# Optimization experiments

Hardware: AMD Instinct MI355X
Metric: run time of the kernel (lower is better)

The kernel has to match this reference:

```python
import jax, jax.numpy as jnp
import numpy as np

B, K, V, T, S, H = 128, 10, 50257, 20, 4, 2048  # batch, beam, vocab, seq_len, n_state, hidden


def setup_inputs() -> dict:
    key = jax.random.key(0)
    k1, k2, k3, k4, k5 = jax.random.split(key, 5)
    return {
        "logprobs": jax.random.normal(k1, (B, K, V), dtype=jnp.float32),
        "logprobs_sum": jax.random.normal(k2, (B, K), dtype=jnp.float32),
        "beam_seq_logprobs": jax.random.normal(k3, (B, T, K), dtype=jnp.float32),
        "state": jax.random.normal(k4, (B, S, K, H), dtype=jnp.float32),
        "beam_seq": jax.random.randint(k5, (B, T, K), 0, V, dtype=jnp.int64),
        "t": 5,
    }


def _beam_step(lp, lp_sum, seq, seq_lp, st, t):
    # lp: [K, V], lp_sum: [K], seq: [T, K] int, seq_lp: [T, K], st: [S, K, H]
    vocab = lp.shape[-1]
    # logprobsf[:, -1] -= 1000 (suppress EOS-like last token)
    lp = lp.at[:, vocab - 1].add(-1000.0)
    # group_size == 1 -> add_diversity is a no-op; unaug_logprobsf == lp.
    # torch.sort(logprobsf, 1, True) then take cols = beam_size per row == per-row top-k
    ys, ix = jax.lax.top_k(lp, K)  # [K(q), K(c)]
    # candidates appended with c outer, q inner -> flat index = c*K + q
    cand = lp_sum[:, None] + ys              # [q, c]
    flat = cand.T.reshape(-1)                # ordered as c*K + q
    order = jnp.argsort(-flat)[:K]           # stable descending sort, keep top beam
    c_sel = order // K
    q_sel = order % K
    tok = ix[q_sel, c_sel]                   # v['c']
    r = ys[q_sel, c_sel]                     # v['r'] (unaug == aug here)
    p = flat[order]                          # v['p']
    time_idx = jnp.arange(seq.shape[0])[:, None]
    # only rows < t are reordered from the parent beam; row t gets new entries
    new_seq = jnp.where(time_idx < t, seq[:, q_sel], seq).at[t].set(tok)
    new_seq_lp = jnp.where(time_idx < t, seq_lp[:, q_sel], seq_lp).at[t].set(r)
    new_state = st[:, q_sel, :]              # state gather/reorder on beam axis
    return new_seq, new_seq_lp, p, new_state


def reference(logprobs, logprobs_sum, beam_seq_logprobs, state, beam_seq, t):
    step = jax.vmap(_beam_step, in_axes=(0, 0, 0, 0, 0, None))
    return step(logprobs, logprobs_sum, beam_seq, beam_seq_logprobs, state, t)
```

## Files before the change

### kernel.cpp

```cpp
#include <hip/hip_runtime.h>
#include <math.h>
#include <stdint.h>

#define NB 128
#define NK 10
#define NV 50257
#define NT 20
#define NS 4
#define NH 2048

#define QCAP 576
#define QTRIG 48

__device__ __forceinline__ unsigned key_of(float f) {
    unsigned u = __float_as_uint(f);
    unsigned m = (unsigned)((int)u >> 31) | 0x80000000u;
    return u ^ m;
}
__device__ __forceinline__ float val_of(unsigned k) {
    unsigned m = (k & 0x80000000u) ? 0x80000000u : 0xFFFFFFFFu;
    return __uint_as_float(k ^ m);
}
__device__ __forceinline__ float rdlanef(float v, int l) {
    return __uint_as_float((unsigned)__builtin_amdgcn_readlane((int)__float_as_uint(v), l));
}

__global__ __launch_bounds__(256) void topk_rows(const float* __restrict__ lp,
                                                 float* __restrict__ ys,
                                                 int*   __restrict__ ix) {
    const int row  = blockIdx.x;
    const int tid  = threadIdx.x;
    const int lane = tid & 63;
    const int wave = tid >> 6;
    const float* rowp = lp + (size_t)row * NV;

    __shared__ unsigned long long Q[4][QCAP];
    __shared__ int qcnt[4];

    if (lane == 0) qcnt[wave] = 0;
    __threadfence_block();

    float thr = -INFINITY;

    auto lane_append = [&](float v, int idx) {
        if (v >= thr) {
            int p = atomicAdd(&qcnt[wave], 1);
            Q[wave][p] = ((unsigned long long)key_of(v) << 32) | (unsigned)(~(unsigned)idx);
        }
    };

    auto compact = [&]() {
        __threadfence_block();
        int cnt = qcnt[wave];
        if (cnt > 10) {
            if (cnt <= 64) {
                unsigned long long mine = (lane < cnt) ? Q[wave][lane] : 0ull;
                int rk = 0;
                for (int j = 0; j < cnt; ++j)
                    rk += (Q[wave][j] > mine) ? 1 : 0;
                __threadfence_block();
                if (lane < cnt && rk < 10) Q[wave][rk] = mine;
            } else {
                unsigned long long mine[9];
                int rk[9];
#pragma unroll
                for (int s = 0; s < 9; ++s) {
                    int e = lane + (s << 6);
                    mine[s] = (e < cnt) ? Q[wave][e] : 0ull;
                    rk[s] = 0;
                }
                for (int j = 0; j < cnt; ++j) {
                    unsigned long long qv = Q[wave][j];
#pragma unroll
                    for (int s = 0; s < 9; ++s) rk[s] += (qv > mine[s]) ? 1 : 0;
                }
                __threadfence_block();
#pragma unroll
                for (int s = 0; s < 9; ++s) {
                    int e = lane + (s << 6);
                    if (e < cnt && rk[s] < 10) Q[wave][rk[s]] = mine[s];
                }
            }
            if (lane == 0) qcnt[wave] = 10;
            __threadfence_block();
            thr = val_of((unsigned)(Q[wave][9] >> 32));
        }
    };

    auto process8 = [&](float4 a, float4 b, int basea) {
        float m8 = fmaxf(fmaxf(fmaxf(a.x, a.y), fmaxf(a.z, a.w)),
                         fmaxf(fmaxf(b.x, b.y), fmaxf(b.z, b.w)));
        if (__ballot(m8 >= thr)) {
            lane_append(a.x, basea + 0);
            lane_append(a.y, basea + 1);
            lane_append(a.z, basea + 2);
            lane_append(a.w, basea + 3);
            lane_append(b.x, basea + 1024);
            lane_append(b.y, basea + 1025);
            lane_append(b.z, basea + 1026);
            lane_append(b.w, basea + 1027);
            __threadfence_block();
            if (qcnt[wave] >= QTRIG) compact();
        }
    };

    const int head = (int)(((16u - (unsigned)((uintptr_t)rowp & 15u)) & 15u) >> 2);
    const int n4 = (NV - 1 - head) >> 2;
    const int NFULL = n4 >> 9;
    const float4* rowp4 = (const float4*)(rowp + head);

    float4 a0 = rowp4[tid];
    float4 b0 = rowp4[tid + 256];
    float4 pa = rowp4[512 + tid];
    float4 pb = rowp4[768 + tid];

    float m8 = fmaxf(fmaxf(fmaxf(a0.x, a0.y), fmaxf(a0.z, a0.w)),
                     fmaxf(fmaxf(b0.x, b0.y), fmaxf(b0.z, b0.w)));
    int rank = 0;
    for (int j = 0; j < 64; ++j) {
        float o = rdlanef(m8, j);
        rank += ((o > m8) || (o == m8 && j < lane)) ? 1 : 0;
    }
    {
        unsigned long long b9 = __ballot(rank == 9);
        int l9 = (int)__builtin_ctzll(b9);
        thr = rdlanef(m8, l9);
    }
    {
        int basea = head + 4 * tid;
        lane_append(a0.x, basea + 0);
        lane_append(a0.y, basea + 1);
        lane_append(a0.z, basea + 2);
        lane_append(a0.w, basea + 3);
        lane_append(b0.x, basea + 1024);
        lane_append(b0.y, basea + 1025);
        lane_append(b0.z, basea + 1026);
        lane_append(b0.w, basea + 1027);
        __threadfence_block();
        if (qcnt[wave] >= QTRIG) compact();
    }

    for (int it = 1; it < NFULL; ++it) {
        float4 ca = pa, cb = pb;
        int nit = (it + 1 < NFULL) ? it + 1 : it;
        pa = rowp4[(nit << 9) + tid];
        pb = rowp4[(nit << 9) + 256 + tid];
        process8(ca, cb, head + 4 * ((it << 9) + tid));
    }
    {
        int ja = (NFULL << 9) + tid;
        int jb = ja + 256;
        float4 a = (ja < n4) ? rowp4[ja]
                             : make_float4(-INFINITY, -INFINITY, -INFINITY, -INFINITY);
        float4 b = (jb < n4) ? rowp4[jb]
                             : make_float4(-INFINITY, -INFINITY, -INFINITY, -INFINITY);
        process8(a, b, head + 4 * ja);
    }
    if (wave == 0) {
        if (lane < head) lane_append(rowp[lane], lane);
        int idx = head + 4 * n4 + lane;
        if (idx < NV) {
            float v = rowp[idx];
            if (idx == NV - 1) v -= 1000.0f;
            lane_append(v, idx);
        }
    }

    compact();
    __syncthreads();

    if (tid < 40) {
        int w = tid / 10, r = tid - w * 10;
        unsigned long long my = Q[w][r];
        int rnk = 0;
#pragma unroll
        for (int w2 = 0; w2 < 4; ++w2)
            for (int r2 = 0; r2 < 10; ++r2)
                rnk += (Q[w2][r2] > my) ? 1 : 0;
        if (rnk < 10) {
            ys[row * 10 + rnk] = val_of((unsigned)(my >> 32));
            ix[row * 10 + rnk] = (int)(~(unsigned)(my & 0xFFFFFFFFull));
        }
    }
}

__global__ __launch_bounds__(128) void beam_select(
    const float* __restrict__ lp_sum,
    const float* __restrict__ seq_lp,
    const int*   __restrict__ seq,
    const int*   __restrict__ tptr,
    const float* __restrict__ ys,
    const int*   __restrict__ ix,
    float* __restrict__ out_seq,
    float* __restrict__ out_seq_lp,
    float* __restrict__ out_p,
    int*   __restrict__ qsel_out)
{
    const int b = blockIdx.x;
    const int tid = threadIdx.x;
    const int t = tptr[0];

    __shared__ float sf[100];
    __shared__ int   so[10];
    __shared__ int   sq[10];
    __shared__ int   stok[10];
    __shared__ float sr[10];

    if (tid < 100) {
        int c = tid / 10, q = tid % 10;
        sf[tid] = lp_sum[b * 10 + q] + ys[(b * 10 + q) * 10 + c];
    }
    __syncthreads();
    if (tid < 100) {
        float v = sf[tid];
        int rank = 0;
        for (int j = 0; j < 100; ++j) {
            float u = sf[j];
            rank += (u > v || (u == v && j < tid)) ? 1 : 0;
        }
        if (rank < 10) so[rank] = tid;
    }
    __syncthreads();
    if (tid < 10) {
        int f = so[tid];
        int c = f / 10, q = f % 10;
        sq[tid] = q;
        stok[tid] = ix[(b * 10 + q) * 10 + c];
        sr[tid] = ys[(b * 10 + q) * 10 + c];
        out_p[b * 10 + tid] = sf[f];
        qsel_out[b * 10 + tid] = q;
    }
    __syncthreads();
    for (int i = tid; i < NT * 10; i += 128) {
        int time = i / 10, k = i % 10;
        int qs = sq[k];
        int src_k = (time < t) ? qs : k;
        int   sval = seq[(b * NT + time) * 10 + src_k];
        float lv = seq_lp[(b * NT + time) * 10 + src_k];
        if (time == t) { sval = stok[k]; lv = sr[k]; }
        out_seq[(b * NT + time) * 10 + k]    = (float)sval;
        out_seq_lp[(b * NT + time) * 10 + k] = lv;
    }
}

__global__ __launch_bounds__(256) void state_gather(
    const float* __restrict__ st,
    const int*   __restrict__ qsel,
    float* __restrict__ out_st)
{
    const int row = blockIdx.x;
    const int k  = row % NK;
    const int bs = row / NK;
    const int b  = bs / NS;
    const int q  = qsel[b * NK + k];

    const float4* src = (const float4*)(st + ((size_t)bs * NK + q) * NH);
    float4*       dst = (float4*)(out_st + (size_t)row * NH);
    const int tid = threadIdx.x;
    dst[tid]       = src[tid];
    dst[tid + 256] = src[tid + 256];
}

extern "C" void kernel_launch(void* const* d_in, const int* in_sizes, int n_in,
                              void* d_out, int out_size, void* d_ws, size_t ws_size,
                              hipStream_t stream) {
    const float* lp      = (const float*)d_in[0];
    const float* lp_sum  = (const float*)d_in[1];
    const float* seq_lp  = (const float*)d_in[2];
    const float* st      = (const float*)d_in[3];
    const int*   seq     = (const int*)d_in[4];
    const int*   tptr    = (const int*)d_in[5];

    float* out        = (float*)d_out;
    float* out_seq    = out;
    float* out_seq_lp = out + NB * NT * NK;
    float* out_p      = out + 2 * NB * NT * NK;
    float* out_st     = out + 2 * NB * NT * NK + NB * NK;

    float* ws_ys   = (float*)d_ws;
    int*   ws_ix   = (int*)((char*)d_ws + 51200);
    int*   ws_qsel = (int*)((char*)d_ws + 102400);

    topk_rows<<<NB * NK, 256, 0, stream>>>(lp, ws_ys, ws_ix);
    beam_select<<<NB, 128, 0, stream>>>(lp_sum, seq_lp, seq, tptr, ws_ys, ws_ix,
                                        out_seq, out_seq_lp, out_p, ws_qsel);
    state_gather<<<NB * NS * NK, 256, 0, stream>>>(st, ws_qsel, out_st);
}
```

Baseline: 69.35 us.

## Fuse beam selection into state gather kernel and skip redundant last-iteration prefetch

Merges the beam_select and state_gather kernels into one launch in which every (batch, state, beam) block recomputes the top-10 candidate ranking locally and then copies its state row. Only one block per batch writes the sequence, logprob and score outputs. This removes a kernel launch and the workspace round trip for the selected parent indices, at the cost of redoing the 100-element ranking 40 times per batch. The top-k loop also stops issuing a duplicate prefetch load on its last iteration.

```diff
diff --git a/kernel.cpp b/kernel.cpp
--- a/kernel.cpp
+++ b/kernel.cpp
@@ -142,9 +142,10 @@
 
     for (int it = 1; it < NFULL; ++it) {
         float4 ca = pa, cb = pb;
-        int nit = (it + 1 < NFULL) ? it + 1 : it;
-        pa = rowp4[(nit << 9) + tid];
-        pb = rowp4[(nit << 9) + 256 + tid];
+        if (it + 1 < NFULL) {
+            pa = rowp4[((it + 1) << 9) + tid];
+            pb = rowp4[((it + 1) << 9) + 256 + tid];
+        }
         process8(ca, cb, head + 4 * ((it << 9) + tid));
     }
     {
@@ -184,21 +185,25 @@
     }
 }
 
-__global__ __launch_bounds__(128) void beam_select(
+__global__ __launch_bounds__(256) void select_gather(
     const float* __restrict__ lp_sum,
     const float* __restrict__ seq_lp,
     const int*   __restrict__ seq,
     const int*   __restrict__ tptr,
     const float* __restrict__ ys,
     const int*   __restrict__ ix,
+    const float* __restrict__ st,
     float* __restrict__ out_seq,
     float* __restrict__ out_seq_lp,
     float* __restrict__ out_p,
-    int*   __restrict__ qsel_out)
+    float* __restrict__ out_st)
 {
-    const int b = blockIdx.x;
+    const int row = blockIdx.x;
+    const int b   = row / (NS * NK);
+    const int rem = row - b * (NS * NK);
+    const int s   = rem / NK;
+    const int k   = rem - s * NK;
     const int tid = threadIdx.x;
-    const int t = tptr[0];
 
     __shared__ float sf[100];
     __shared__ int   so[10];
@@ -221,44 +226,35 @@
         if (rank < 10) so[rank] = tid;
     }
     __syncthreads();
-    if (tid < 10) {
-        int f = so[tid];
-        int c = f / 10, q = f % 10;
-        sq[tid] = q;
-        stok[tid] = ix[(b * 10 + q) * 10 + c];
-        sr[tid] = ys[(b * 10 + q) * 10 + c];
-        out_p[b * 10 + tid] = sf[f];
-        qsel_out[b * 10 + tid] = q;
-    }
-    __syncthreads();
-    for (int i = tid; i < NT * 10; i += 128) {
-        int time = i / 10, k = i % 10;
-        int qs = sq[k];
-        int src_k = (time < t) ? qs : k;
-        int   sval = seq[(b * NT + time) * 10 + src_k];
-        float lv = seq_lp[(b * NT + time) * 10 + src_k];
-        if (time == t) { sval = stok[k]; lv = sr[k]; }
-        out_seq[(b * NT + time) * 10 + k]    = (float)sval;
-        out_seq_lp[(b * NT + time) * 10 + k] = lv;
-    }
-}
-
-__global__ __launch_bounds__(256) void state_gather(
-    const float* __restrict__ st,
-    const int*   __restrict__ qsel,
-    float* __restrict__ out_st)
-{
-    const int row = blockIdx.x;
-    const int k  = row % NK;
-    const int bs = row / NK;
-    const int b  = bs / NS;
-    const int q  = qsel[b * NK + k];
-
-    const float4* src = (const float4*)(st + ((size_t)bs * NK + q) * NH);
+
+    const int q = so[k] % 10;
+    const float4* src = (const float4*)(st + ((size_t)(b * NS + s) * NK + q) * NH);
     float4*       dst = (float4*)(out_st + (size_t)row * NH);
-    const int tid = threadIdx.x;
     dst[tid]       = src[tid];
     dst[tid + 256] = src[tid + 256];
+
+    if (s == 0 && k == 0) {
+        const int t = tptr[0];
+        if (tid < 10) {
+            int f = so[tid];
+            int c = f / 10, qq = f % 10;
+            sq[tid]   = qq;
+            stok[tid] = ix[(b * 10 + qq) * 10 + c];
+            sr[tid]   = ys[(b * 10 + qq) * 10 + c];
+            out_p[b * 10 + tid] = sf[f];
+        }
+        __syncthreads();
+        if (tid < NT * NK) {
+            int time = tid / 10, kk = tid % 10;
+            int qs = sq[kk];
+            int src_k = (time < t) ? qs : kk;
+            int   sval = seq[(b * NT + time) * 10 + src_k];
+            float lv = seq_lp[(b * NT + time) * 10 + src_k];
+            if (time == t) { sval = stok[kk]; lv = sr[kk]; }
+            out_seq[(b * NT + time) * 10 + kk]    = (float)sval;
+            out_seq_lp[(b * NT + time) * 10 + kk] = lv;
+        }
+    }
 }
 
 extern "C" void kernel_launch(void* const* d_in, const int* in_sizes, int n_in,
@@ -279,10 +275,9 @@
 
     float* ws_ys   = (float*)d_ws;
     int*   ws_ix   = (int*)((char*)d_ws + 51200);
-    int*   ws_qsel = (int*)((char*)d_ws + 102400);
 
     topk_rows<<<NB * NK, 256, 0, stream>>>(lp, ws_ys, ws_ix);
-    beam_select<<<NB, 128, 0, stream>>>(lp_sum, seq_lp, seq, tptr, ws_ys, ws_ix,
-                                        out_seq, out_seq_lp, out_p, ws_qsel);
-    state_gather<<<NB * NS * NK, 256, 0, stream>>>(st, ws_qsel, out_st);
-}
+    select_gather<<<NB * NS * NK, 256, 0, stream>>>(
+        lp_sum, seq_lp, seq, tptr, ws_ys, ws_ix, st,
+        out_seq, out_seq_lp, out_p, out_st);
+}
```

Result: no change. 68.93 us (-0.6%).
